# Optimization experiments

Measured on AMD Instinct MI355X. Metric: run time of the kernel, lower is better.

The kernel has to match this reference:

```python
import jax, jax.numpy as jnp
import numpy as np

F = 16384   # n_features
D = 768     # d_model
B = 2       # batch
S = 256     # seq len
C = 16      # connections per downstream feature
M = F * C   # total connections


def setup_inputs() -> dict:
    key = jax.random.key(0)
    k1, k2, k3, k4 = jax.random.split(key, 4)
    up_facts = jax.random.normal(k1, (B, S, F), dtype=jnp.float32)
    down_encoder = jax.random.normal(k2, (F, D), dtype=jnp.float32) * 0.02
    up_decoder = jax.random.normal(k3, (D, F), dtype=jnp.float32) * 0.02
    # connection_mask.nonzero() is row-major: i sorted, C targets per row
    i_indices = jnp.repeat(jnp.arange(F, dtype=jnp.int32), C)  # [M]
    j_indices = jax.random.randint(k4, (M,), 0, F, dtype=jnp.int32)  # [M]
    return {
        "up_facts": up_facts,
        "down_encoder": down_encoder,
        "up_decoder": up_decoder,
        "i_indices": i_indices,
        "j_indices": j_indices,
    }


def reference(up_facts, down_encoder, up_decoder, i_indices, j_indices):
    # up_facts: [B,S,F]; down_encoder: [F,D]; up_decoder: [D,F]
    b, s, f = up_facts.shape
    m = i_indices.shape[0]
    # per-connection virtual weight: values[m] = down_encoder[i[m]] . up_decoder[:, j[m]]
    values = jnp.einsum("md,dm->m", down_encoder[i_indices], up_decoder[:, j_indices])  # [M]
    # gather upstream feature activations and scale
    scaled = up_facts[:, :, j_indices] * values[None, None, :]  # [B,S,M]
    # scatter_add over last axis into downstream feature bins (i is constant across B,S)
    flat = scaled.reshape(b * s, m).T  # [M, B*S]
    contrib = jax.ops.segment_sum(flat, i_indices, num_segments=f)  # [F, B*S]
    return contrib.T.reshape(b, s, f)
```

## Files before the change

### kernel.cpp

```cpp
#include <hip/hip_runtime.h>
#include <hip/hip_bf16.h>

#define F_ 16384
#define D_ 768
#define C_ 16
#define BS_ 512
#define M_ (F_*C_)

static __device__ __forceinline__ float bf2f(unsigned short u) {
    return __uint_as_float(((unsigned int)u) << 16);
}

__global__ __launch_bounds__(256) void k_transpose_bf16(const float* __restrict__ in,
                                                        unsigned short* __restrict__ out) {
    __shared__ float tile[64][33];
    int tx = threadIdx.x & 31;
    int ty = threadIdx.x >> 5;
    int fcol = blockIdx.x * 32 + tx;
#pragma unroll
    for (int r = 0; r < 64; r += 8) {
        int drow = blockIdx.y * 64 + ty + r;
        tile[ty + r][tx] = in[(size_t)drow * F_ + fcol];
    }
    __syncthreads();
    int dp = threadIdx.x & 31;
    int fy = threadIdx.x >> 5;
#pragma unroll
    for (int r = 0; r < 32; r += 8) {
        int frow_l = fy + r;
        float v0 = tile[2 * dp][frow_l];
        float v1 = tile[2 * dp + 1][frow_l];
        unsigned int p = ((unsigned int)(__bfloat16_as_ushort(__float2bfloat16(v1))) << 16)
                       |  (unsigned int)(__bfloat16_as_ushort(__float2bfloat16(v0)));
        int frow = blockIdx.x * 32 + frow_l;
        unsigned int* o = (unsigned int*)(out + (size_t)frow * D_ + blockIdx.y * 64);
        o[dp] = p;
    }
}

__global__ __launch_bounds__(256) void k_values(const float* __restrict__ enc,
                                                const unsigned short* __restrict__ decT,
                                                const int* __restrict__ jidx,
                                                float* __restrict__ values) {
    int f = blockIdx.x;
    int lane = threadIdx.x & 63;
    int wave = threadIdx.x >> 6;
    const float4* erow = (const float4*)(enc + (size_t)f * D_);
    float4 e[3];
    e[0] = erow[lane];
    e[1] = erow[lane + 64];
    e[2] = erow[lane + 128];
    int4 j4 = *(const int4*)(jidx + (f << 4) + (wave << 2));
    int js[4] = {j4.x, j4.y, j4.z, j4.w};
    ushort4 g[4][3];
#pragma unroll
    for (int t = 0; t < 4; ++t) {
        const ushort4* drow = (const ushort4*)(decT + (size_t)js[t] * D_);
        g[t][0] = drow[lane];
        g[t][1] = drow[lane + 64];
        g[t][2] = drow[lane + 128];
    }
#pragma unroll
    for (int t = 0; t < 4; ++t) {
        float acc = 0.f;
#pragma unroll
        for (int k = 0; k < 3; ++k) {
            float4 ev = e[k];
            ushort4 dv = g[t][k];
            acc += ev.x * bf2f(dv.x) + ev.y * bf2f(dv.y)
                 + ev.z * bf2f(dv.z) + ev.w * bf2f(dv.w);
        }
#pragma unroll
        for (int off = 32; off > 0; off >>= 1)
            acc += __shfl_down(acc, off, 64);
        if (lane == 0) values[(f << 4) + (wave << 2) + t] = acc;
    }
}

__global__ __launch_bounds__(1024) void k_out(const float* __restrict__ up,
                                              const int* __restrict__ jidx,
                                              const float* __restrict__ values,
                                              float* __restrict__ out) {
    __shared__ unsigned int rowp[F_];
    int bs0 = blockIdx.x << 1;
    const float4* u0 = (const float4*)(up + (size_t)bs0 * F_);
    const float4* u1 = (const float4*)(up + (size_t)(bs0 + 1) * F_);
#pragma unroll
    for (int t = 0; t < 4; ++t) {
        int idx = threadIdx.x + t * 1024;
        float4 a = u0[idx];
        float4 b = u1[idx];
        uint4 p;
        p.x = ((unsigned int)__bfloat16_as_ushort(__float2bfloat16(b.x)) << 16)
            |  (unsigned int)__bfloat16_as_ushort(__float2bfloat16(a.x));
        p.y = ((unsigned int)__bfloat16_as_ushort(__float2bfloat16(b.y)) << 16)
            |  (unsigned int)__bfloat16_as_ushort(__float2bfloat16(a.y));
        p.z = ((unsigned int)__bfloat16_as_ushort(__float2bfloat16(b.z)) << 16)
            |  (unsigned int)__bfloat16_as_ushort(__float2bfloat16(a.z));
        p.w = ((unsigned int)__bfloat16_as_ushort(__float2bfloat16(b.w)) << 16)
            |  (unsigned int)__bfloat16_as_ushort(__float2bfloat16(a.w));
        ((uint4*)rowp)[idx] = p;
    }
    __syncthreads();
#pragma unroll
    for (int it = 0; it < 16; ++it) {
        int f = threadIdx.x + it * 1024;
        const int4*   jp = (const int4*)(jidx + ((size_t)f << 4));
        const float4* vp = (const float4*)(values + ((size_t)f << 4));
        float a0 = 0.f, a1 = 0.f;
#pragma unroll
        for (int q = 0; q < 4; ++q) {
            int4   j4 = jp[q];
            float4 v4 = vp[q];
            unsigned int px = rowp[j4.x];
            unsigned int py = rowp[j4.y];
            unsigned int pz = rowp[j4.z];
            unsigned int pw = rowp[j4.w];
            a0 += bf2f((unsigned short)(px & 0xffff)) * v4.x
                + bf2f((unsigned short)(py & 0xffff)) * v4.y
                + bf2f((unsigned short)(pz & 0xffff)) * v4.z
                + bf2f((unsigned short)(pw & 0xffff)) * v4.w;
            a1 += bf2f((unsigned short)(px >> 16)) * v4.x
                + bf2f((unsigned short)(py >> 16)) * v4.y
                + bf2f((unsigned short)(pz >> 16)) * v4.z
                + bf2f((unsigned short)(pw >> 16)) * v4.w;
        }
        out[(size_t)bs0 * F_ + f] = a0;
        out[(size_t)(bs0 + 1) * F_ + f] = a1;
    }
}

extern "C" void kernel_launch(void* const* d_in, const int* in_sizes, int n_in,
                              void* d_out, int out_size, void* d_ws, size_t ws_size,
                              hipStream_t stream) {
    const float* up   = (const float*)d_in[0];
    const float* enc  = (const float*)d_in[1];
    const float* dec  = (const float*)d_in[2];
    const int*   jidx = (const int*)d_in[4];
    float*       out  = (float*)d_out;

    size_t decT_bytes = (size_t)F_ * D_ * sizeof(unsigned short);
    unsigned short* decT = (unsigned short*)d_ws;
    float* values = (float*)((char*)d_ws + decT_bytes);

    k_transpose_bf16<<<dim3(F_ / 32, D_ / 64), 256, 0, stream>>>(dec, decT);
    k_values<<<F_, 256, 0, stream>>>(enc, decT, jidx, values);
    k_out<<<BS_ / 2, 1024, 0, stream>>>(up, jidx, values, out);
}
```

Baseline: 245.2 us.

## Pack bf16 value with 16-bit index and split output kernel across two blocks

Each connection's weight is now rounded to bf16 and packed with its 16-bit j index into one 32-bit word. The output kernel then streams a single packed array instead of separate int and float arrays, halving per-connection metadata traffic. The output kernel now runs twice as many 512-thread blocks, each covering half the features for a pair of rows, which adds parallelism but loads and converts the same up_facts row pair twice. The transpose is widened to float4 loads and 64x64 tiles with 8-byte stores. Rounding the connection weights to bf16 loses some precision.

```diff
diff --git a/kernel.cpp b/kernel.cpp
--- a/kernel.cpp
+++ b/kernel.cpp
@@ -10,38 +10,47 @@
 static __device__ __forceinline__ float bf2f(unsigned short u) {
     return __uint_as_float(((unsigned int)u) << 16);
 }
+static __device__ __forceinline__ unsigned short f2bf(float f) {
+    return __bfloat16_as_ushort(__float2bfloat16(f));
+}
 
 __global__ __launch_bounds__(256) void k_transpose_bf16(const float* __restrict__ in,
                                                         unsigned short* __restrict__ out) {
-    __shared__ float tile[64][33];
-    int tx = threadIdx.x & 31;
-    int ty = threadIdx.x >> 5;
-    int fcol = blockIdx.x * 32 + tx;
+    __shared__ float tile[64][65];
+    int c4 = threadIdx.x & 15;
+    int r  = threadIdx.x >> 4;
+    int fbase = blockIdx.x * 64;
+    int dbase = blockIdx.y * 64;
 #pragma unroll
-    for (int r = 0; r < 64; r += 8) {
-        int drow = blockIdx.y * 64 + ty + r;
-        tile[ty + r][tx] = in[(size_t)drow * F_ + fcol];
+    for (int k = 0; k < 4; ++k) {
+        int drow = r + k * 16;
+        float4 v = *(const float4*)(in + (size_t)(dbase + drow) * F_ + fbase + c4 * 4);
+        tile[drow][c4 * 4 + 0] = v.x;
+        tile[drow][c4 * 4 + 1] = v.y;
+        tile[drow][c4 * 4 + 2] = v.z;
+        tile[drow][c4 * 4 + 3] = v.w;
     }
     __syncthreads();
-    int dp = threadIdx.x & 31;
-    int fy = threadIdx.x >> 5;
+    int dp = threadIdx.x & 15;
+    int fr = threadIdx.x >> 4;
 #pragma unroll
-    for (int r = 0; r < 32; r += 8) {
-        int frow_l = fy + r;
-        float v0 = tile[2 * dp][frow_l];
-        float v1 = tile[2 * dp + 1][frow_l];
-        unsigned int p = ((unsigned int)(__bfloat16_as_ushort(__float2bfloat16(v1))) << 16)
-                       |  (unsigned int)(__bfloat16_as_ushort(__float2bfloat16(v0)));
-        int frow = blockIdx.x * 32 + frow_l;
-        unsigned int* o = (unsigned int*)(out + (size_t)frow * D_ + blockIdx.y * 64);
-        o[dp] = p;
+    for (int k = 0; k < 4; ++k) {
+        int frow = fr + k * 16;
+        float v0 = tile[4 * dp + 0][frow];
+        float v1 = tile[4 * dp + 1][frow];
+        float v2 = tile[4 * dp + 2][frow];
+        float v3 = tile[4 * dp + 3][frow];
+        uint2 p;
+        p.x = ((unsigned int)f2bf(v1) << 16) | (unsigned int)f2bf(v0);
+        p.y = ((unsigned int)f2bf(v3) << 16) | (unsigned int)f2bf(v2);
+        *(uint2*)(out + (size_t)(fbase + frow) * D_ + dbase + dp * 4) = p;
     }
 }
 
 __global__ __launch_bounds__(256) void k_values(const float* __restrict__ enc,
                                                 const unsigned short* __restrict__ decT,
                                                 const int* __restrict__ jidx,
-                                                float* __restrict__ values) {
+                                                unsigned int* __restrict__ packed) {
     int f = blockIdx.x;
     int lane = threadIdx.x & 63;
     int wave = threadIdx.x >> 6;
@@ -73,57 +82,48 @@
 #pragma unroll
         for (int off = 32; off > 0; off >>= 1)
             acc += __shfl_down(acc, off, 64);
-        if (lane == 0) values[(f << 4) + (wave << 2) + t] = acc;
+        if (lane == 0)
+            packed[(f << 4) + (wave << 2) + t] =
+                ((unsigned int)f2bf(acc) << 16) | (unsigned int)js[t];
     }
 }
 
-__global__ __launch_bounds__(1024) void k_out(const float* __restrict__ up,
-                                              const int* __restrict__ jidx,
-                                              const float* __restrict__ values,
-                                              float* __restrict__ out) {
+__global__ __launch_bounds__(512) void k_out(const float* __restrict__ up,
+                                             const unsigned int* __restrict__ packed,
+                                             float* __restrict__ out) {
     __shared__ unsigned int rowp[F_];
-    int bs0 = blockIdx.x << 1;
+    int bs0  = (blockIdx.x >> 1) << 1;
+    int half = blockIdx.x & 1;
     const float4* u0 = (const float4*)(up + (size_t)bs0 * F_);
     const float4* u1 = (const float4*)(up + (size_t)(bs0 + 1) * F_);
 #pragma unroll
-    for (int t = 0; t < 4; ++t) {
-        int idx = threadIdx.x + t * 1024;
+    for (int k = 0; k < 8; ++k) {
+        int idx = threadIdx.x + k * 512;
         float4 a = u0[idx];
         float4 b = u1[idx];
         uint4 p;
-        p.x = ((unsigned int)__bfloat16_as_ushort(__float2bfloat16(b.x)) << 16)
-            |  (unsigned int)__bfloat16_as_ushort(__float2bfloat16(a.x));
-        p.y = ((unsigned int)__bfloat16_as_ushort(__float2bfloat16(b.y)) << 16)
-            |  (unsigned int)__bfloat16_as_ushort(__float2bfloat16(a.y));
-        p.z = ((unsigned int)__bfloat16_as_ushort(__float2bfloat16(b.z)) << 16)
-            |  (unsigned int)__bfloat16_as_ushort(__float2bfloat16(a.z));
-        p.w = ((unsigned int)__bfloat16_as_ushort(__float2bfloat16(b.w)) << 16)
-            |  (unsigned int)__bfloat16_as_ushort(__float2bfloat16(a.w));
+        p.x = ((unsigned int)f2bf(b.x) << 16) | (unsigned int)f2bf(a.x);
+        p.y = ((unsigned int)f2bf(b.y) << 16) | (unsigned int)f2bf(a.y);
+        p.z = ((unsigned int)f2bf(b.z) << 16) | (unsigned int)f2bf(a.z);
+        p.w = ((unsigned int)f2bf(b.w) << 16) | (unsigned int)f2bf(a.w);
         ((uint4*)rowp)[idx] = p;
     }
     __syncthreads();
-#pragma unroll
+    int f0 = half << 13;
+#pragma unroll 4
     for (int it = 0; it < 16; ++it) {
-        int f = threadIdx.x + it * 1024;
-        const int4*   jp = (const int4*)(jidx + ((size_t)f << 4));
-        const float4* vp = (const float4*)(values + ((size_t)f << 4));
+        int f = f0 + threadIdx.x + it * 512;
+        const uint4* sp = (const uint4*)(packed + ((size_t)f << 4));
         float a0 = 0.f, a1 = 0.f;
 #pragma unroll
         for (int q = 0; q < 4; ++q) {
-            int4   j4 = jp[q];
-            float4 v4 = vp[q];
-            unsigned int px = rowp[j4.x];
-            unsigned int py = rowp[j4.y];
-            unsigned int pz = rowp[j4.z];
-            unsigned int pw = rowp[j4.w];
-            a0 += bf2f((unsigned short)(px & 0xffff)) * v4.x
-                + bf2f((unsigned short)(py & 0xffff)) * v4.y
-                + bf2f((unsigned short)(pz & 0xffff)) * v4.z
-                + bf2f((unsigned short)(pw & 0xffff)) * v4.w;
-            a1 += bf2f((unsigned short)(px >> 16)) * v4.x
-                + bf2f((unsigned short)(py >> 16)) * v4.y
-                + bf2f((unsigned short)(pz >> 16)) * v4.z
-                + bf2f((unsigned short)(pw >> 16)) * v4.w;
+            uint4 w = sp[q];
+#define CONN(ww) { unsigned int p_ = rowp[(ww) & 0xffffu];                  \
+                   float v_ = __uint_as_float((ww) & 0xffff0000u);          \
+                   a0 += __uint_as_float(p_ << 16) * v_;                    \
+                   a1 += __uint_as_float(p_ & 0xffff0000u) * v_; }
+            CONN(w.x) CONN(w.y) CONN(w.z) CONN(w.w)
+#undef CONN
         }
         out[(size_t)bs0 * F_ + f] = a0;
         out[(size_t)(bs0 + 1) * F_ + f] = a1;
@@ -140,10 +140,10 @@
     float*       out  = (float*)d_out;
 
     size_t decT_bytes = (size_t)F_ * D_ * sizeof(unsigned short);
-    unsigned short* decT = (unsigned short*)d_ws;
-    float* values = (float*)((char*)d_ws + decT_bytes);
+    unsigned short* decT   = (unsigned short*)d_ws;
+    unsigned int*   packed = (unsigned int*)((char*)d_ws + decT_bytes);
 
-    k_transpose_bf16<<<dim3(F_ / 32, D_ / 64), 256, 0, stream>>>(dec, decT);
-    k_values<<<F_, 256, 0, stream>>>(enc, decT, jidx, values);
-    k_out<<<BS_ / 2, 1024, 0, stream>>>(up, jidx, values, out);
+    k_transpose_bf16<<<dim3(F_ / 64, D_ / 64), 256, 0, stream>>>(dec, decT);
+    k_values<<<F_, 256, 0, stream>>>(enc, decT, jidx, packed);
+    k_out<<<BS_, 512, 0, stream>>>(up, packed, out);
 }
```

New measurement: 222.9 us. -9.1%, faster.
